# Optimization experiments

Measured on AMD Instinct MI355X. Metric: run time of the kernel, lower is better.

The kernel has to match this reference:

```python
import jax, jax.numpy as jnp
import numpy as np

N, E, F, DE, G, C = 50000, 800000, 64, 32, 512, 2
EPS = 1e-5


def setup_inputs() -> dict:
    key = jax.random.key(0)
    ks = jax.random.split(key, 12)
    Z = 2 * F + DE  # CGConv concat dim [x_i, x_j, edge_attr]
    inp = {
        "x": jax.random.normal(ks[0], (N, F), dtype=jnp.float32),
        "edge_index": jax.random.randint(ks[1], (2, E), 0, N, dtype=jnp.int32),
        "edge_attr": jax.random.normal(ks[2], (E, DE), dtype=jnp.float32),
        "batch": jnp.sort(jax.random.randint(ks[3], (N,), 0, G, dtype=jnp.int32)),
        # CGConv lin_f / lin_s : (2F+De) -> F, with bias
        "Wf": jax.random.normal(ks[4], (Z, F), dtype=jnp.float32) * 0.05,
        "bf": jnp.zeros((F,), dtype=jnp.float32),
        "Ws": jax.random.normal(ks[5], (Z, F), dtype=jnp.float32) * 0.05,
        "bs": jnp.zeros((F,), dtype=jnp.float32),
        # CGConv internal BatchNorm (training-mode batch stats)
        "bn_w": jnp.ones((F,), dtype=jnp.float32),
        "bn_b": jnp.zeros((F,), dtype=jnp.float32),
        # PyG LayerNorm (graph mode, batch=None -> whole-tensor stats)
        "ln_w": jnp.ones((F,), dtype=jnp.float32),
        "ln_b": jnp.zeros((F,), dtype=jnp.float32),
        # final linear (2F -> C) and output LayerNorm
        "Wl": jax.random.normal(ks[6], (2 * F, C), dtype=jnp.float32) * 0.05,
        "bl": jnp.zeros((C,), dtype=jnp.float32),
        "ln4_w": jnp.ones((C,), dtype=jnp.float32),
        "ln4_b": jnp.zeros((C,), dtype=jnp.float32),
    }
    return inp


def _pyg_layernorm(x, w, b):
    # torch_geometric.nn.LayerNorm, mode='graph', batch=None: whole-tensor stats
    xc = x - jnp.mean(x)
    out = xc / (jnp.sqrt(jnp.mean(xc * xc)) + EPS)
    return out * w + b


def reference(x, edge_index, edge_attr, batch, Wf, bf, Ws, bs, bn_w, bn_b,
              ln_w, ln_b, Wl, bl, ln4_w, ln4_b):
    src = edge_index[0]  # x_j (source)
    dst = edge_index[1]  # x_i (target / aggregation index)

    # CGConv message: sigmoid(lin_f(z)) * softplus(lin_s(z)), z=[x_i,x_j,e]
    z = jnp.concatenate([x[dst], x[src], edge_attr], axis=1)  # [E, 2F+De]
    msg = jax.nn.sigmoid(z @ Wf + bf) * jax.nn.softplus(z @ Ws + bs)  # [E,F]

    # scatter-add aggregation to target nodes
    agg = jax.ops.segment_sum(msg, dst, num_segments=N)  # [N,F]

    # CGConv batch_norm=True (training-mode batch statistics over nodes)
    mu = jnp.mean(agg, axis=0)
    var = jnp.mean((agg - mu) ** 2, axis=0)
    agg = (agg - mu) / jnp.sqrt(var + EPS) * bn_w + bn_b

    # residual
    h = agg + x

    # LayerNorm + softplus
    h = jax.nn.softplus(_pyg_layernorm(h, ln_w, ln_b))

    # global mean / add pooling over graphs
    add_pool = jax.ops.segment_sum(h, batch, num_segments=G)  # [G,F]
    counts = jax.ops.segment_sum(jnp.ones((N,), h.dtype), batch, num_segments=G)
    mean_pool = add_pool / jnp.maximum(counts, 1.0)[:, None]

    g = jnp.concatenate([mean_pool, add_pool], axis=1)  # [G, 2F]
    out = g @ Wl + bl  # [G, C]
    out = _pyg_layernorm(out, ln4_w, ln4_b)
    return out
```

## Files before the change

kernel.cpp:

```cpp
#include <hip/hip_runtime.h>
#include <math.h>

#define EPSF 1e-5f

typedef short bf16x8 __attribute__((ext_vector_type(8)));
typedef float f32x4 __attribute__((ext_vector_type(4)));

static __device__ __forceinline__ unsigned short f2bf(float x) {
  unsigned u = __float_as_uint(x);
  unsigned r = (u + 0x7FFFu + ((u >> 16) & 1u)) >> 16;
  return (unsigned short)r;
}

union BU { uint4 u; bf16x8 v; };

static __device__ __forceinline__ void gload16(const void* g, void* l) {
  __builtin_amdgcn_global_load_lds(
      (const __attribute__((address_space(1))) unsigned int*)g,
      (__attribute__((address_space(3))) unsigned int*)l, 16, 0, 0);
}

__global__ __launch_bounds__(256) void cvt_x(const float* __restrict__ x,
                                             unsigned short* __restrict__ xbf,
                                             int total8) {
  int i = blockIdx.x * 256 + threadIdx.x;
  if (i >= total8) return;
  float4 a = ((const float4*)x)[i * 2];
  float4 b = ((const float4*)x)[i * 2 + 1];
  unsigned short o[8];
  o[0] = f2bf(a.x); o[1] = f2bf(a.y); o[2] = f2bf(a.z); o[3] = f2bf(a.w);
  o[4] = f2bf(b.x); o[5] = f2bf(b.y); o[6] = f2bf(b.z); o[7] = f2bf(b.w);
  ((uint4*)xbf)[i] = *(uint4*)o;
}

__global__ __launch_bounds__(512) void bpack_kernel(
    const float* __restrict__ Wf, const float* __restrict__ Ws,
    unsigned short* __restrict__ Bfrag) {
  const int ks = blockIdx.x;
  const int t8 = threadIdx.x >> 6, l = threadIdx.x & 63;
  const int q = l & 15, g = l >> 4;
  const float* W = (t8 < 4) ? Wf : Ws;
  const int col = (t8 & 3) * 16 + q;
  unsigned short out[8];
#pragma unroll
  for (int i = 0; i < 8; ++i) {
    int r = ks * 32 + g * 8 + i;
    int wr = (r < 32) ? (128 + r) : (r - 32);
    out[i] = f2bf(W[(size_t)wr * 64 + col]);
  }
  *(uint4*)&Bfrag[((size_t)(ks * 8 + t8) * 64 + l) * 8] = *(uint4*)out;
}

__global__ void hist_kernel(const int* __restrict__ ei, int* __restrict__ deg,
                            int E) {
  int i = blockIdx.x * blockDim.x + threadIdx.x;
  if (i < E) atomicAdd(&deg[ei[E + i]], 1);
}

__global__ __launch_bounds__(256) void scan_a(const int* __restrict__ deg,
                                              int* __restrict__ bsum, int N) {
  const int idx = blockIdx.x * 256 + threadIdx.x;
  int v = (idx < N) ? deg[idx] : 0;
#pragma unroll
  for (int o = 32; o > 0; o >>= 1) v += __shfl_down(v, o);
  __shared__ int ws4[4];
  if ((threadIdx.x & 63) == 0) ws4[threadIdx.x >> 6] = v;
  __syncthreads();
  if (threadIdx.x == 0) bsum[blockIdx.x] = ws4[0] + ws4[1] + ws4[2] + ws4[3];
}

__global__ __launch_bounds__(256) void scan_b(const int* __restrict__ bsum,
                                              int* __restrict__ bpre, int NB) {
  const int t = threadIdx.x;
  const int lane = t & 63, w = t >> 6;
  int v = (t < NB) ? bsum[t] : 0;
  int sc = v;
#pragma unroll
  for (int o = 1; o < 64; o <<= 1) {
    int u = __shfl_up(sc, o);
    if (lane >= o) sc += u;
  }
  __shared__ int wsum[4];
  if (lane == 63) wsum[w] = sc;
  __syncthreads();
  int add = 0;
#pragma unroll
  for (int k = 0; k < 4; ++k) add += (k < w) ? wsum[k] : 0;
  bpre[t] = (sc - v) + add;
}

__global__ __launch_bounds__(256) void scan_c(const int* __restrict__ deg,
                                              const int* __restrict__ bpre,
                                              int* __restrict__ offsets,
                                              int* __restrict__ cursor, int N) {
  const int t = threadIdx.x;
  const int lane = t & 63, w = t >> 6;
  const int idx = blockIdx.x * 256 + t;
  int d = (idx < N) ? deg[idx] : 0;
  int sc = d;
#pragma unroll
  for (int o = 1; o < 64; o <<= 1) {
    int u = __shfl_up(sc, o);
    if (lane >= o) sc += u;
  }
  __shared__ int wsum[4];
  if (lane == 63) wsum[w] = sc;
  __syncthreads();
  int add = bpre[blockIdx.x];
#pragma unroll
  for (int k = 0; k < 4; ++k) add += (k < w) ? wsum[k] : 0;
  const int off = add + (sc - d);
  if (idx < N) {
    offsets[idx] = off;
    cursor[idx] = off;
    if (idx == N - 1) offsets[N] = off + d;
  }
}

__global__ void scatter_kernel(const int* __restrict__ ei,
                               int* __restrict__ cursor,
                               int4* __restrict__ epair4, int E) {
  int i = blockIdx.x * blockDim.x + threadIdx.x;
  if (i < E) {
    int dst = ei[E + i];
    int pos = atomicAdd(&cursor[dst], 1);
    epair4[pos] = make_int4(i, ei[i], dst, 0);
  }
}

__global__ __launch_bounds__(256) void edge_fused(
    const int4* __restrict__ epair4, const float* __restrict__ eattr,
    const unsigned short* __restrict__ xbf,
    const unsigned short* __restrict__ Bfrag, const float* __restrict__ bfv_,
    const float* __restrict__ bsv_, float* __restrict__ agg, int E, int N) {
  __shared__ __align__(16) unsigned short Ash[5][64][32];
  __shared__ __align__(16) int srcl[64];
  __shared__ __align__(16) int dstl[64];
  __shared__ __align__(16) int eidx[64];
  __shared__ __align__(4) unsigned char ridb[64];

  const int t = threadIdx.x, lane = t & 63, w = t >> 6;
  const int q = lane & 15, g = lane >> 4;
  const int base = blockIdx.x * 64;

  bf16x8 Bf[5], Bs[5];
#pragma unroll
  for (int ks = 0; ks < 5; ++ks) {
    BU u1, u2;
    u1.u = ((const uint4*)Bfrag)[(size_t)((ks * 8 + w) * 64 + lane)];
    u2.u = ((const uint4*)Bfrag)[(size_t)((ks * 8 + w + 4) * 64 + lane)];
    Bf[ks] = u1.v;
    Bs[ks] = u2.v;
  }
  const int feat = w * 16 + q;
  const float bfv = bfv_[feat];
  const float bsv = bsv_[feat];

  if (w == 0) {
    const int eg = base + lane;
    int4 p = make_int4(0, 0, 0x7FFFFFFF, 0);
    if (eg < E) p = epair4[eg];
    eidx[lane] = p.x;
    srcl[lane] = p.y;
    dstl[lane] = p.z;
    int d = p.z;
    int dprev = __shfl_up(d, 1);
    int flag = (lane == 0 || d != dprev) ? 1 : 0;
    int sc = flag;
#pragma unroll
    for (int o = 1; o < 64; o <<= 1) {
      int u = __shfl_up(sc, o);
      if (lane >= o) sc += u;
    }
    ridb[lane] = (unsigned char)(sc - 1);
  }
  __syncthreads();

  char* AshB = (char*)&Ash[0][0][0];
#pragma unroll
  for (int c2 = 0; c2 < 2; ++c2) {
    const int k = w + c2 * 4;
    const int row = 16 * (k & 3) + (lane >> 2);
    const int half = (k >> 2) * 32 + (lane & 3) * 8;
    int d = dstl[row];
    if ((unsigned)d >= (unsigned)N) d = 0;
    gload16(xbf + (size_t)d * 64 + half, AshB + 4096 + (size_t)k * 1024);
    const int s = srcl[row];
    gload16(xbf + (size_t)s * 64 + half, AshB + 12288 + (size_t)k * 1024);
  }

  {
    const int row = t >> 2, c = t & 3;
    const float* er = eattr + (size_t)eidx[row] * 32 + c * 8;
    float4 v0 = *(const float4*)er;
    float4 v1 = *(const float4*)(er + 4);
    bf16x8 sv;
    sv[0] = (short)f2bf(v0.x); sv[1] = (short)f2bf(v0.y);
    sv[2] = (short)f2bf(v0.z); sv[3] = (short)f2bf(v0.w);
    sv[4] = (short)f2bf(v1.x); sv[5] = (short)f2bf(v1.y);
    sv[6] = (short)f2bf(v1.z); sv[7] = (short)f2bf(v1.w);
    *(bf16x8*)&Ash[0][row][c * 8] = sv;
  }
  __syncthreads();

  f32x4 accf[4], accs[4];
#pragma unroll
  for (int mt = 0; mt < 4; ++mt) {
    accf[mt] = (f32x4){0.f, 0.f, 0.f, 0.f};
    accs[mt] = (f32x4){0.f, 0.f, 0.f, 0.f};
  }
#pragma unroll
  for (int ks = 0; ks < 5; ++ks) {
#pragma unroll
    for (int mt = 0; mt < 4; ++mt) {
      const bf16x8 a = *(const bf16x8*)&Ash[ks][mt * 16 + q][g * 8];
      accf[mt] =
          __builtin_amdgcn_mfma_f32_16x16x32_bf16(a, Bf[ks], accf[mt], 0, 0, 0);
      accs[mt] =
          __builtin_amdgcn_mfma_f32_16x16x32_bf16(a, Bs[ks], accs[mt], 0, 0, 0);
    }
  }

#pragma unroll
  for (int mt = 0; mt < 4; ++mt) {
    const int e0 = mt * 16 + g * 4;
    const unsigned rid4 = *(const unsigned*)&ridb[e0];
    const int4 d4 = *(const int4*)&dstl[e0];
    float m[4];
#pragma unroll
    for (int r = 0; r < 4; ++r) {
      float F = accf[mt][r] + bfv;
      float S = accs[mt][r] + bsv;
      float sig = __builtin_amdgcn_rcpf(1.0f + __expf(-F));
      float sp = fmaxf(S, 0.f) + __logf(1.0f + __expf(-fabsf(S)));
      m[r] = sig * sp;
    }
    const int r0 = rid4 & 255, r1 = (rid4 >> 8) & 255, r2 = (rid4 >> 16) & 255,
              r3 = rid4 >> 24;
    float a_ = m[0];
    int cur = r0, dc = d4.x;
    if (r1 == cur) a_ += m[1];
    else {
      if (dc < N) atomicAdd(&agg[(size_t)dc * 64 + feat], a_);
      cur = r1; dc = d4.y; a_ = m[1];
    }
    if (r2 == cur) a_ += m[2];
    else {
      if (dc < N) atomicAdd(&agg[(size_t)dc * 64 + feat], a_);
      cur = r2; dc = d4.z; a_ = m[2];
    }
    if (r3 == cur) a_ += m[3];
    else {
      if (dc < N) atomicAdd(&agg[(size_t)dc * 64 + feat], a_);
      cur = r3; dc = d4.w; a_ = m[3];
    }
    if (dc < N) atomicAdd(&agg[(size_t)dc * 64 + feat], a_);
  }
}

__global__ __launch_bounds__(256) void stats_kernel(
    const float* __restrict__ agg, const float* __restrict__ x,
    float* __restrict__ stats, int N) {
  const int f = threadIdx.x & 63;
  const int sub = threadIdx.x >> 6;
  float sa = 0, sa2 = 0, sx = 0, sx2 = 0, sax = 0;
  for (int r = blockIdx.x * 4 + sub; r < N; r += gridDim.x * 4) {
    float a = agg[(size_t)r * 64 + f];
    float xv = x[(size_t)r * 64 + f];
    sa += a; sa2 += a * a; sx += xv; sx2 += xv * xv; sax += a * xv;
  }
  __shared__ float lds[4][5][64];
  lds[sub][0][f] = sa; lds[sub][1][f] = sa2; lds[sub][2][f] = sx;
  lds[sub][3][f] = sx2; lds[sub][4][f] = sax;
  __syncthreads();
  if (sub == 0) {
#pragma unroll
    for (int i = 0; i < 5; ++i) {
      float v = lds[0][i][f] + lds[1][i][f] + lds[2][i][f] + lds[3][i][f];
      atomicAdd(&stats[i * 64 + f], v);
    }
  }
}

__global__ __launch_bounds__(256) void node_finish(
    const float* __restrict__ stats, const float* __restrict__ bn_w,
    const float* __restrict__ bn_b, const float* __restrict__ agg,
    const float* __restrict__ x, const int* __restrict__ batch,
    const float* __restrict__ ln_w, const float* __restrict__ ln_b,
    float* __restrict__ add_pool, float* __restrict__ counts, int N,
    int chunk) {
  const int f = threadIdx.x & 63;
  const int sub = threadIdx.x >> 6;
  const float Nf = (float)N;
  const float invN = 1.0f / Nf;
  float Sa = stats[f], Sa2 = stats[64 + f], Sx = stats[128 + f],
        Sx2 = stats[192 + f], Sax = stats[256 + f];
  float mu = Sa * invN;
  float var = Sa2 * invN - mu * mu;
  const float alpha = bn_w[f] / sqrtf(var + EPSF);
  const float beta = bn_b[f] - mu * alpha;
  float Sh = alpha * Sa + Nf * beta + Sx;
  float Sh2 = alpha * alpha * Sa2 + Sx2 + Nf * beta * beta +
              2.f * alpha * Sax + 2.f * alpha * beta * Sa + 2.f * beta * Sx;
#pragma unroll
  for (int o = 32; o > 0; o >>= 1) {
    Sh += __shfl_xor(Sh, o);
    Sh2 += __shfl_xor(Sh2, o);
  }
  const float cnt = Nf * 64.0f;
  const float mean = Sh / cnt;
  const float msq = Sh2 / cnt - mean * mean;
  const float rden = 1.0f / (sqrtf(fmaxf(msq, 0.f)) + EPSF);
  const float lw = ln_w[f] * rden;
  const float lb = ln_b[f];

  const int r0 = blockIdx.x * chunk;
  const int r1 = min(N, r0 + chunk);
  float acc = 0.f, cacc = 0.f;
  int curg = -1;
  for (int r = r0 + sub; r < r1; r += 4) {
    int g = batch[r];
    if (g != curg) {
      if (curg >= 0) {
        atomicAdd(&add_pool[(size_t)curg * 64 + f], acc);
        if (f == 0) atomicAdd(&counts[curg], cacc);
      }
      curg = g; acc = 0.f; cacc = 0.f;
    }
    float h = fmaf(alpha, agg[(size_t)r * 64 + f], beta) + x[(size_t)r * 64 + f];
    float v = (h - mean) * lw + lb;
    float sp = fmaxf(v, 0.f) + __logf(1.0f + __expf(-fabsf(v)));
    acc += sp; cacc += 1.f;
  }
  if (curg >= 0) {
    atomicAdd(&add_pool[(size_t)curg * 64 + f], acc);
    if (f == 0) atomicAdd(&counts[curg], cacc);
  }
}

__global__ __launch_bounds__(1024) void graph_out(
    const float* __restrict__ add_pool, const float* __restrict__ counts,
    const float* __restrict__ Wl, const float* __restrict__ bl,
    const float* __restrict__ w4, const float* __restrict__ b4,
    float* __restrict__ out, int G) {
  const int t = threadIdx.x;
  const int g = t >> 1, c = t & 1;
  float cnt = fmaxf(counts[g], 1.0f);
  float inv = 1.0f / cnt;
  const float4* ap4 = (const float4*)(add_pool + (size_t)g * 64);
  const float4* W4 = (const float4*)Wl;
  float v = bl[c];
#pragma unroll 4
  for (int k4 = 0; k4 < 16; ++k4) {
    float4 a4 = ap4[k4];
    float4 wa = W4[k4 * 2];
    float4 wb = W4[k4 * 2 + 1];
    float4 wc = W4[32 + k4 * 2];
    float4 wd = W4[32 + k4 * 2 + 1];
    float m0 = c ? wa.y : wa.x, m1 = c ? wa.w : wa.z;
    float m2 = c ? wb.y : wb.x, m3 = c ? wb.w : wb.z;
    float a0 = c ? wc.y : wc.x, a1 = c ? wc.w : wc.z;
    float a2 = c ? wd.y : wd.x, a3 = c ? wd.w : wd.z;
    v = fmaf(a4.x, fmaf(m0, inv, a0), v);
    v = fmaf(a4.y, fmaf(m1, inv, a1), v);
    v = fmaf(a4.z, fmaf(m2, inv, a2), v);
    v = fmaf(a4.w, fmaf(m3, inv, a3), v);
  }

  __shared__ float red[16];
  __shared__ float bc[2];
  float sum = v;
#pragma unroll
  for (int o = 32; o > 0; o >>= 1) sum += __shfl_down(sum, o);
  if ((t & 63) == 0) red[t >> 6] = sum;
  __syncthreads();
  if (t == 0) {
    float tot = 0;
#pragma unroll
    for (int i = 0; i < 16; ++i) tot += red[i];
    bc[0] = tot * (1.0f / 1024.0f);
  }
  __syncthreads();
  const float mean = bc[0];
  const float xc = v - mean;
  float sq = xc * xc;
  __syncthreads();
#pragma unroll
  for (int o = 32; o > 0; o >>= 1) sq += __shfl_down(sq, o);
  if ((t & 63) == 0) red[t >> 6] = sq;
  __syncthreads();
  if (t == 0) {
    float tot = 0;
#pragma unroll
    for (int i = 0; i < 16; ++i) tot += red[i];
    bc[1] = 1.0f / (sqrtf(tot * (1.0f / 1024.0f)) + EPSF);
  }
  __syncthreads();
  out[t] = xc * bc[1] * w4[c] + b4[c];
}

extern "C" void kernel_launch(void* const* d_in, const int* in_sizes, int n_in,
                              void* d_out, int out_size, void* d_ws,
                              size_t ws_size, hipStream_t stream) {
  const float* x = (const float*)d_in[0];
  const int* ei = (const int*)d_in[1];
  const float* eattr = (const float*)d_in[2];
  const int* batch = (const int*)d_in[3];
  const float* Wf = (const float*)d_in[4];
  const float* bf = (const float*)d_in[5];
  const float* Ws = (const float*)d_in[6];
  const float* bs = (const float*)d_in[7];
  const float* bn_w = (const float*)d_in[8];
  const float* bn_b = (const float*)d_in[9];
  const float* ln_w = (const float*)d_in[10];
  const float* ln_b = (const float*)d_in[11];
  const float* Wl = (const float*)d_in[12];
  const float* bl = (const float*)d_in[13];
  const float* w4 = (const float*)d_in[14];
  const float* b4 = (const float*)d_in[15];

  const int N = in_sizes[0] / 64;
  const int E = in_sizes[2] / 32;
  const int G = 512;
  const int NB = (N + 255) / 256;
  const int T = (E + 63) / 64;

  float* ws = (float*)d_ws;
  float* agg = ws;
  float* stats = agg + (size_t)N * 64;
  float* add_pool = stats + 320;
  float* counts = add_pool + (size_t)G * 64;
  int* deg = (int*)(counts + G);
  int* offsets = deg + N;
  int* cursor = offsets + N + 4;
  int* bsum = cursor + N;
  int* bpre = bsum + 256;
  unsigned short* Bfrag = (unsigned short*)(bpre + 256);
  unsigned short* xbf = Bfrag + 20480;
  int4* epair4 = (int4*)(xbf + (size_t)N * 64);

  size_t zeroFloats = (size_t)N * 64 + 320 + (size_t)G * 64 + G + N;
  hipMemsetAsync(agg, 0, zeroFloats * sizeof(float), stream);

  cvt_x<<<(N * 64 / 8 + 255) / 256, 256, 0, stream>>>(x, xbf, N * 64 / 8);
  bpack_kernel<<<5, 512, 0, stream>>>(Wf, Ws, Bfrag);
  hist_kernel<<<(E + 255) / 256, 256, 0, stream>>>(ei, deg, E);
  scan_a<<<NB, 256, 0, stream>>>(deg, bsum, N);
  scan_b<<<1, 256, 0, stream>>>(bsum, bpre, NB);
  scan_c<<<NB, 256, 0, stream>>>(deg, bpre, offsets, cursor, N);
  scatter_kernel<<<(E + 255) / 256, 256, 0, stream>>>(ei, cursor, epair4, E);
  edge_fused<<<T, 256, 0, stream>>>(epair4, eattr, xbf, Bfrag, bf, bs, agg, E,
                                    N);
  stats_kernel<<<512, 256, 0, stream>>>(agg, x, stats, N);
  const int chunk = (N + 511) / 512;
  node_finish<<<512, 256, 0, stream>>>(stats, bn_w, bn_b, agg, x, batch, ln_w,
                                       ln_b, add_pool, counts, N, chunk);
  graph_out<<<1, 1024, 0, stream>>>(add_pool, counts, Wl, bl, w4, b4,
                                    (float*)d_out, G);
}
```

Before: 328.7 us.

## Persistent double-buffered edge kernel with pre-sorted bf16 edge attributes and fused prep

Merges the x conversion, weight packing and degree histogram into one prep launch. The scatter step now writes edge attributes to bf16 in sorted order, so the edge kernel loads them contiguously with async LDS loads instead of gathering fp32 rows. The edge kernel becomes persistent with a fixed 768-block grid: each block walks a contiguous run of tiles and prefetches the next tile's metadata and operands into a second LDS buffer while computing the current one. It also adds an XOR swizzle to the LDS layout to avoid bank conflicts. In exchange it uses more LDS per block and adds extra scatter work, and it assumes node ids fit in 20 bits.

Result: no change. 329.2 us (+0.2%).

```diff
diff --git a/kernel.cpp b/kernel.cpp
--- a/kernel.cpp
+++ b/kernel.cpp
@@ -20,41 +20,42 @@
       (__attribute__((address_space(3))) unsigned int*)l, 16, 0, 0);
 }
 
-__global__ __launch_bounds__(256) void cvt_x(const float* __restrict__ x,
-                                             unsigned short* __restrict__ xbf,
-                                             int total8) {
-  int i = blockIdx.x * 256 + threadIdx.x;
-  if (i >= total8) return;
-  float4 a = ((const float4*)x)[i * 2];
-  float4 b = ((const float4*)x)[i * 2 + 1];
-  unsigned short o[8];
-  o[0] = f2bf(a.x); o[1] = f2bf(a.y); o[2] = f2bf(a.z); o[3] = f2bf(a.w);
-  o[4] = f2bf(b.x); o[5] = f2bf(b.y); o[6] = f2bf(b.z); o[7] = f2bf(b.w);
-  ((uint4*)xbf)[i] = *(uint4*)o;
-}
-
-__global__ __launch_bounds__(512) void bpack_kernel(
-    const float* __restrict__ Wf, const float* __restrict__ Ws,
-    unsigned short* __restrict__ Bfrag) {
-  const int ks = blockIdx.x;
-  const int t8 = threadIdx.x >> 6, l = threadIdx.x & 63;
-  const int q = l & 15, g = l >> 4;
-  const float* W = (t8 < 4) ? Wf : Ws;
-  const int col = (t8 & 3) * 16 + q;
-  unsigned short out[8];
-#pragma unroll
-  for (int i = 0; i < 8; ++i) {
-    int r = ks * 32 + g * 8 + i;
-    int wr = (r < 32) ? (128 + r) : (r - 32);
-    out[i] = f2bf(W[(size_t)wr * 64 + col]);
-  }
-  *(uint4*)&Bfrag[((size_t)(ks * 8 + t8) * 64 + l) * 8] = *(uint4*)out;
-}
-
-__global__ void hist_kernel(const int* __restrict__ ei, int* __restrict__ deg,
-                            int E) {
-  int i = blockIdx.x * blockDim.x + threadIdx.x;
-  if (i < E) atomicAdd(&deg[ei[E + i]], 1);
+__global__ __launch_bounds__(256) void prep_kernel(
+    const float* __restrict__ x, const float* __restrict__ Wf,
+    const float* __restrict__ Ws, const int* __restrict__ ei,
+    unsigned short* __restrict__ xbf, unsigned short* __restrict__ Bfrag,
+    int* __restrict__ deg, int NCV, int total8, int E) {
+  const int b = blockIdx.x, t = threadIdx.x;
+  if (b < NCV) {
+    int i = b * 256 + t;
+    if (i < total8) {
+      float4 a = ((const float4*)x)[i * 2];
+      float4 c = ((const float4*)x)[i * 2 + 1];
+      unsigned short o[8];
+      o[0] = f2bf(a.x); o[1] = f2bf(a.y); o[2] = f2bf(a.z); o[3] = f2bf(a.w);
+      o[4] = f2bf(c.x); o[5] = f2bf(c.y); o[6] = f2bf(c.z); o[7] = f2bf(c.w);
+      ((uint4*)xbf)[i] = *(uint4*)o;
+    }
+  } else if (b < NCV + 10) {
+    int g2 = (b - NCV) * 256 + t;
+    if (g2 < 2560) {
+      const int ks = g2 >> 9, t8 = (g2 >> 6) & 7, l = g2 & 63;
+      const int q = l & 15, g = l >> 4;
+      const float* W = (t8 < 4) ? Wf : Ws;
+      const int col = (t8 & 3) * 16 + q;
+      unsigned short out[8];
+#pragma unroll
+      for (int i = 0; i < 8; ++i) {
+        int r = ks * 32 + g * 8 + i;
+        int wr = (r < 32) ? (128 + r) : (r - 32);
+        out[i] = f2bf(W[(size_t)wr * 64 + col]);
+      }
+      *(uint4*)&Bfrag[((size_t)(ks * 8 + t8) * 64 + l) * 8] = *(uint4*)out;
+    }
+  } else {
+    int i = (b - NCV - 10) * 256 + t;
+    if (i < E) atomicAdd(&deg[ei[E + i]], 1);
+  }
 }
 
 __global__ __launch_bounds__(256) void scan_a(const int* __restrict__ deg,
@@ -91,7 +92,6 @@
 
 __global__ __launch_bounds__(256) void scan_c(const int* __restrict__ deg,
                                               const int* __restrict__ bpre,
-                                              int* __restrict__ offsets,
                                               int* __restrict__ cursor, int N) {
   const int t = threadIdx.x;
   const int lane = t & 63, w = t >> 6;
@@ -109,152 +109,170 @@
   int add = bpre[blockIdx.x];
 #pragma unroll
   for (int k = 0; k < 4; ++k) add += (k < w) ? wsum[k] : 0;
-  const int off = add + (sc - d);
-  if (idx < N) {
-    offsets[idx] = off;
-    cursor[idx] = off;
-    if (idx == N - 1) offsets[N] = off + d;
-  }
-}
-
-__global__ void scatter_kernel(const int* __restrict__ ei,
-                               int* __restrict__ cursor,
-                               int4* __restrict__ epair4, int E) {
-  int i = blockIdx.x * blockDim.x + threadIdx.x;
-  if (i < E) {
-    int dst = ei[E + i];
-    int pos = atomicAdd(&cursor[dst], 1);
-    epair4[pos] = make_int4(i, ei[i], dst, 0);
-  }
-}
-
-__global__ __launch_bounds__(256) void edge_fused(
-    const int4* __restrict__ epair4, const float* __restrict__ eattr,
+  if (idx < N) cursor[idx] = add + (sc - d);
+}
+
+__global__ __launch_bounds__(256) void scatter_pack(
+    const int* __restrict__ ei, int* __restrict__ cursor,
+    const float* __restrict__ eattr, int2* __restrict__ epair2,
+    unsigned short* __restrict__ eabf, int E) {
+  int i = blockIdx.x * 256 + threadIdx.x;
+  if (i >= E) return;
+  const int dst = ei[E + i];
+  const int pos = atomicAdd(&cursor[dst], 1);
+  epair2[pos] = make_int2(ei[i], dst);
+  const float4* er = (const float4*)(eattr + (size_t)i * 32);
+  unsigned short o[32];
+#pragma unroll
+  for (int k = 0; k < 8; ++k) {
+    float4 v = er[k];
+    o[k * 4] = f2bf(v.x); o[k * 4 + 1] = f2bf(v.y);
+    o[k * 4 + 2] = f2bf(v.z); o[k * 4 + 3] = f2bf(v.w);
+  }
+  uint4* dp = (uint4*)(eabf + (size_t)pos * 32);
+#pragma unroll
+  for (int k = 0; k < 4; ++k) dp[k] = ((uint4*)o)[k];
+}
+
+__global__ __launch_bounds__(256, 3) void edge_fused(
+    const int2* __restrict__ epair2, const unsigned short* __restrict__ eabf,
     const unsigned short* __restrict__ xbf,
     const unsigned short* __restrict__ Bfrag, const float* __restrict__ bfv_,
-    const float* __restrict__ bsv_, float* __restrict__ agg, int E, int N) {
-  __shared__ __align__(16) unsigned short Ash[5][64][32];
-  __shared__ __align__(16) int srcl[64];
-  __shared__ __align__(16) int dstl[64];
-  __shared__ __align__(16) int eidx[64];
-  __shared__ __align__(4) unsigned char ridb[64];
-
-  const int t = threadIdx.x, lane = t & 63, w = t >> 6;
+    const float* __restrict__ bsv_, float* __restrict__ agg, int T, int N) {
+  __shared__ __align__(16) unsigned char AshB[40960];
+  __shared__ __align__(16) int metaLDS[128];
+
+  const int tt = threadIdx.x, lane = tt & 63, w = tt >> 6;
   const int q = lane & 15, g = lane >> 4;
-  const int base = blockIdx.x * 64;
+
+  const int nB = gridDim.x;
+  const int c = (blockIdx.x & 7) * (nB >> 3) + (blockIdx.x >> 3);
+  const int q8 = T / nB, r8 = T - q8 * nB;
+  const int t0 = c * q8 + min(c, r8);
+  const int t1 = t0 + q8 + (c < r8 ? 1 : 0);
+  if (t0 >= t1) return;
 
   bf16x8 Bf[5], Bs[5];
 #pragma unroll
   for (int ks = 0; ks < 5; ++ks) {
     BU u1, u2;
-    u1.u = ((const uint4*)Bfrag)[(size_t)((ks * 8 + w) * 64 + lane)];
-    u2.u = ((const uint4*)Bfrag)[(size_t)((ks * 8 + w + 4) * 64 + lane)];
-    Bf[ks] = u1.v;
-    Bs[ks] = u2.v;
+    u1.u = ((const uint4*)Bfrag)[(ks * 8 + w) * 64 + lane];
+    u2.u = ((const uint4*)Bfrag)[(ks * 8 + w + 4) * 64 + lane];
+    Bf[ks] = u1.v; Bs[ks] = u2.v;
   }
   const int feat = w * 16 + q;
-  const float bfv = bfv_[feat];
-  const float bsv = bsv_[feat];
-
-  if (w == 0) {
-    const int eg = base + lane;
-    int4 p = make_int4(0, 0, 0x7FFFFFFF, 0);
-    if (eg < E) p = epair4[eg];
-    eidx[lane] = p.x;
-    srcl[lane] = p.y;
-    dstl[lane] = p.z;
-    int d = p.z;
-    int dprev = __shfl_up(d, 1);
-    int flag = (lane == 0 || d != dprev) ? 1 : 0;
+  const float bfv = bfv_[feat], bsv = bsv_[feat];
+
+  int mSrc = 0, mDst = 0, nSrc = 0, nDst = 0;
+
+  auto META = [&](int tile, int& S, int& D, int pbN) {
+    int2 p = epair2[(size_t)tile * 64 + lane];
+    S = p.x; D = p.y;
+    int dp = __shfl_up(D, 1);
+    int flag = (lane == 0 || D != dp) ? 1 : 0;
     int sc = flag;
 #pragma unroll
     for (int o = 1; o < 64; o <<= 1) {
       int u = __shfl_up(sc, o);
       if (lane >= o) sc += u;
     }
-    ridb[lane] = (unsigned char)(sc - 1);
-  }
-  __syncthreads();
-
-  char* AshB = (char*)&Ash[0][0][0];
-#pragma unroll
-  for (int c2 = 0; c2 < 2; ++c2) {
-    const int k = w + c2 * 4;
-    const int row = 16 * (k & 3) + (lane >> 2);
-    const int half = (k >> 2) * 32 + (lane & 3) * 8;
-    int d = dstl[row];
-    if ((unsigned)d >= (unsigned)N) d = 0;
-    gload16(xbf + (size_t)d * 64 + half, AshB + 4096 + (size_t)k * 1024);
-    const int s = srcl[row];
-    gload16(xbf + (size_t)s * 64 + half, AshB + 12288 + (size_t)k * 1024);
-  }
-
-  {
-    const int row = t >> 2, c = t & 3;
-    const float* er = eattr + (size_t)eidx[row] * 32 + c * 8;
-    float4 v0 = *(const float4*)er;
-    float4 v1 = *(const float4*)(er + 4);
-    bf16x8 sv;
-    sv[0] = (short)f2bf(v0.x); sv[1] = (short)f2bf(v0.y);
-    sv[2] = (short)f2bf(v0.z); sv[3] = (short)f2bf(v0.w);
-    sv[4] = (short)f2bf(v1.x); sv[5] = (short)f2bf(v1.y);
-    sv[6] = (short)f2bf(v1.z); sv[7] = (short)f2bf(v1.w);
-    *(bf16x8*)&Ash[0][row][c * 8] = sv;
-  }
-  __syncthreads();
-
-  f32x4 accf[4], accs[4];
-#pragma unroll
-  for (int mt = 0; mt < 4; ++mt) {
-    accf[mt] = (f32x4){0.f, 0.f, 0.f, 0.f};
-    accs[mt] = (f32x4){0.f, 0.f, 0.f, 0.f};
-  }
-#pragma unroll
-  for (int ks = 0; ks < 5; ++ks) {
+    if (w == 0) metaLDS[pbN * 64 + lane] = ((sc - 1) << 20) | (D & 0xFFFFF);
+  };
+
+  auto STAGE = [&](int tile, int bufB, int S, int D) {
+    const int row = (w << 4) + (lane >> 2);
+    const int cx = (lane & 3) ^ ((row >> 1) & 3);
+    int dR = __shfl(D, row);
+    int sR = __shfl(S, row);
+    unsigned du = ((unsigned)dR < (unsigned)N) ? (unsigned)dR : 0u;
+    unsigned su = ((unsigned)sR < (unsigned)N) ? (unsigned)sR : 0u;
+    gload16(eabf + (size_t)tile * 2048 + row * 32 + cx * 8,
+            AshB + bufB + w * 1024);
+    gload16(xbf + (size_t)du * 64 + cx * 8, AshB + bufB + 4096 + w * 1024);
+    gload16(xbf + (size_t)du * 64 + 32 + cx * 8,
+            AshB + bufB + 4096 + (w + 4) * 1024);
+    gload16(xbf + (size_t)su * 64 + cx * 8, AshB + bufB + 12288 + w * 1024);
+    gload16(xbf + (size_t)su * 64 + 32 + cx * 8,
+            AshB + bufB + 12288 + (w + 4) * 1024);
+  };
+
+  META(t0, mSrc, mDst, 0);
+  STAGE(t0, 0, mSrc, mDst);
+  int pb = 0;
+  for (int t = t0; t < t1; ++t) {
+    const int bufC = pb * 20480;
+    if (t + 1 < t1) {
+      META(t + 1, nSrc, nDst, pb ^ 1);
+      STAGE(t + 1, 20480 - bufC, nSrc, nDst);
+    } else {
+      asm volatile("s_waitcnt vmcnt(0)" ::: "memory");
+    }
+    asm volatile("s_waitcnt lgkmcnt(0)" ::: "memory");
+    __builtin_amdgcn_sched_barrier(0);
+    __builtin_amdgcn_s_barrier();
+    __builtin_amdgcn_sched_barrier(0);
+
+    f32x4 accf[4], accs[4];
 #pragma unroll
     for (int mt = 0; mt < 4; ++mt) {
-      const bf16x8 a = *(const bf16x8*)&Ash[ks][mt * 16 + q][g * 8];
-      accf[mt] =
-          __builtin_amdgcn_mfma_f32_16x16x32_bf16(a, Bf[ks], accf[mt], 0, 0, 0);
-      accs[mt] =
-          __builtin_amdgcn_mfma_f32_16x16x32_bf16(a, Bs[ks], accs[mt], 0, 0, 0);
-    }
-  }
-
-#pragma unroll
-  for (int mt = 0; mt < 4; ++mt) {
-    const int e0 = mt * 16 + g * 4;
-    const unsigned rid4 = *(const unsigned*)&ridb[e0];
-    const int4 d4 = *(const int4*)&dstl[e0];
-    float m[4];
-#pragma unroll
-    for (int r = 0; r < 4; ++r) {
-      float F = accf[mt][r] + bfv;
-      float S = accs[mt][r] + bsv;
-      float sig = __builtin_amdgcn_rcpf(1.0f + __expf(-F));
-      float sp = fmaxf(S, 0.f) + __logf(1.0f + __expf(-fabsf(S)));
-      m[r] = sig * sp;
-    }
-    const int r0 = rid4 & 255, r1 = (rid4 >> 8) & 255, r2 = (rid4 >> 16) & 255,
-              r3 = rid4 >> 24;
-    float a_ = m[0];
-    int cur = r0, dc = d4.x;
-    if (r1 == cur) a_ += m[1];
-    else {
-      if (dc < N) atomicAdd(&agg[(size_t)dc * 64 + feat], a_);
-      cur = r1; dc = d4.y; a_ = m[1];
-    }
-    if (r2 == cur) a_ += m[2];
-    else {
-      if (dc < N) atomicAdd(&agg[(size_t)dc * 64 + feat], a_);
-      cur = r2; dc = d4.z; a_ = m[2];
-    }
-    if (r3 == cur) a_ += m[3];
-    else {
-      if (dc < N) atomicAdd(&agg[(size_t)dc * 64 + feat], a_);
-      cur = r3; dc = d4.w; a_ = m[3];
-    }
-    if (dc < N) atomicAdd(&agg[(size_t)dc * 64 + feat], a_);
+      accf[mt] = (f32x4){0.f, 0.f, 0.f, 0.f};
+      accs[mt] = (f32x4){0.f, 0.f, 0.f, 0.f};
+    }
+#pragma unroll
+    for (int ks = 0; ks < 5; ++ks) {
+#pragma unroll
+      for (int mt = 0; mt < 4; ++mt) {
+        const int row = mt * 16 + q;
+        const int ch = g ^ ((row >> 1) & 3);
+        const bf16x8 a =
+            *(const bf16x8*)(AshB + bufC + ks * 4096 + row * 64 + ch * 16);
+        accf[mt] = __builtin_amdgcn_mfma_f32_16x16x32_bf16(a, Bf[ks],
+                                                           accf[mt], 0, 0, 0);
+        accs[mt] = __builtin_amdgcn_mfma_f32_16x16x32_bf16(a, Bs[ks],
+                                                           accs[mt], 0, 0, 0);
+      }
+    }
+
+#pragma unroll
+    for (int mt = 0; mt < 4; ++mt) {
+      const int e0 = mt * 16 + g * 4;
+      const uint4 mw = *(const uint4*)&metaLDS[pb * 64 + e0];
+      float mm[4];
+#pragma unroll
+      for (int r = 0; r < 4; ++r) {
+        float F = accf[mt][r] + bfv;
+        float S = accs[mt][r] + bsv;
+        float sig = __builtin_amdgcn_rcpf(1.0f + __expf(-F));
+        float sp = fmaxf(S, 0.f) + __logf(1.0f + __expf(-fabsf(S)));
+        mm[r] = sig * sp;
+      }
+      const unsigned u0 = mw.x, u1 = mw.y, u2 = mw.z, u3 = mw.w;
+      const unsigned d0 = u0 & 0xFFFFFu, d1 = u1 & 0xFFFFFu,
+                     d2 = u2 & 0xFFFFFu, d3 = u3 & 0xFFFFFu;
+      const unsigned r0 = u0 >> 20, r1 = u1 >> 20, r2 = u2 >> 20, r3 = u3 >> 20;
+      float a_ = mm[0];
+      unsigned cur = r0, dc = d0;
+      if (r1 == cur) a_ += mm[1];
+      else {
+        if (dc < (unsigned)N) atomicAdd(&agg[(size_t)dc * 64 + feat], a_);
+        cur = r1; dc = d1; a_ = mm[1];
+      }
+      if (r2 == cur) a_ += mm[2];
+      else {
+        if (dc < (unsigned)N) atomicAdd(&agg[(size_t)dc * 64 + feat], a_);
+        cur = r2; dc = d2; a_ = mm[2];
+      }
+      if (r3 == cur) a_ += mm[3];
+      else {
+        if (dc < (unsigned)N) atomicAdd(&agg[(size_t)dc * 64 + feat], a_);
+        cur = r3; dc = d3; a_ = mm[3];
+      }
+      if (dc < (unsigned)N) atomicAdd(&agg[(size_t)dc * 64 + feat], a_);
+    }
+
+    mSrc = nSrc; mDst = nDst;
+    pb ^= 1;
+    __builtin_amdgcn_s_barrier();
   }
 }
 
@@ -424,6 +442,8 @@
   const int G = 512;
   const int NB = (N + 255) / 256;
   const int T = (E + 63) / 64;
+  const int NCV = (N * 8 + 255) / 256;
+  const int NH = (E + 255) / 256;
 
   float* ws = (float*)d_ws;
   float* agg = ws;
@@ -431,26 +451,27 @@
   float* add_pool = stats + 320;
   float* counts = add_pool + (size_t)G * 64;
   int* deg = (int*)(counts + G);
-  int* offsets = deg + N;
-  int* cursor = offsets + N + 4;
+  int* cursor = deg + N;
   int* bsum = cursor + N;
   int* bpre = bsum + 256;
   unsigned short* Bfrag = (unsigned short*)(bpre + 256);
   unsigned short* xbf = Bfrag + 20480;
-  int4* epair4 = (int4*)(xbf + (size_t)N * 64);
+  unsigned short* eabf = xbf + (size_t)N * 64;
+  int2* epair2 = (int2*)(eabf + (size_t)T * 2048);
 
   size_t zeroFloats = (size_t)N * 64 + 320 + (size_t)G * 64 + G + N;
   hipMemsetAsync(agg, 0, zeroFloats * sizeof(float), stream);
-
-  cvt_x<<<(N * 64 / 8 + 255) / 256, 256, 0, stream>>>(x, xbf, N * 64 / 8);
-  bpack_kernel<<<5, 512, 0, stream>>>(Wf, Ws, Bfrag);
-  hist_kernel<<<(E + 255) / 256, 256, 0, stream>>>(ei, deg, E);
+  const int padE = T * 64 - E;
+  if (padE > 0) hipMemsetAsync(epair2 + E, 0xFF, (size_t)padE * 8, stream);
+
+  prep_kernel<<<NCV + 10 + NH, 256, 0, stream>>>(x, Wf, Ws, ei, xbf, Bfrag,
+                                                 deg, NCV, N * 8, E);
   scan_a<<<NB, 256, 0, stream>>>(deg, bsum, N);
   scan_b<<<1, 256, 0, stream>>>(bsum, bpre, NB);
-  scan_c<<<NB, 256, 0, stream>>>(deg, bpre, offsets, cursor, N);
-  scatter_kernel<<<(E + 255) / 256, 256, 0, stream>>>(ei, cursor, epair4, E);
-  edge_fused<<<T, 256, 0, stream>>>(epair4, eattr, xbf, Bfrag, bf, bs, agg, E,
-                                    N);
+  scan_c<<<NB, 256, 0, stream>>>(deg, bpre, cursor, N);
+  scatter_pack<<<NH, 256, 0, stream>>>(ei, cursor, eattr, epair2, eabf, E);
+  edge_fused<<<768, 256, 0, stream>>>(epair2, eabf, xbf, Bfrag, bf, bs, agg, T,
+                                      N);
   stats_kernel<<<512, 256, 0, stream>>>(agg, x, stats, N);
   const int chunk = (N + 511) / 512;
   node_finish<<<512, 256, 0, stream>>>(stats, bn_w, bn_b, agg, x, batch, ln_w,
```

## Merge prep kernels and restructure edge gather with swizzled LDS and early loads

Applied to the files above, without the earlier changes.

Folds the x bf16 conversion, weight-fragment packing and degree histogram into one multi-role launch, and drops the unused offsets array. In the edge kernel, each thread now reads its own edge record and issues the x-row and edge-attribute gathers before the weight-fragment loads and the first barrier, which removes one barrier and the LDS index arrays. LDS A-tiles use an XOR swizzle on the 16-byte chunks to cut bank conflicts. The tail of the sorted edge array is padded with 0xFF via memset so out-of-range edges are skipped by unsigned bounds checks.

After: 320.2 us. -2.6%, faster.

```diff
diff --git a/kernel.cpp b/kernel.cpp
--- a/kernel.cpp
+++ b/kernel.cpp
@@ -12,6 +12,12 @@
   return (unsigned short)r;
 }
 
+static __device__ __forceinline__ float msgv(float F, float S) {
+  float sig = __builtin_amdgcn_rcpf(1.0f + __expf(-F));
+  float sp = fmaxf(S, 0.f) + __logf(1.0f + __expf(-fabsf(S)));
+  return sig * sp;
+}
+
 union BU { uint4 u; bf16x8 v; };
 
 static __device__ __forceinline__ void gload16(const void* g, void* l) {
@@ -20,41 +26,42 @@
       (__attribute__((address_space(3))) unsigned int*)l, 16, 0, 0);
 }
 
-__global__ __launch_bounds__(256) void cvt_x(const float* __restrict__ x,
-                                             unsigned short* __restrict__ xbf,
-                                             int total8) {
-  int i = blockIdx.x * 256 + threadIdx.x;
-  if (i >= total8) return;
-  float4 a = ((const float4*)x)[i * 2];
-  float4 b = ((const float4*)x)[i * 2 + 1];
-  unsigned short o[8];
-  o[0] = f2bf(a.x); o[1] = f2bf(a.y); o[2] = f2bf(a.z); o[3] = f2bf(a.w);
-  o[4] = f2bf(b.x); o[5] = f2bf(b.y); o[6] = f2bf(b.z); o[7] = f2bf(b.w);
-  ((uint4*)xbf)[i] = *(uint4*)o;
-}
-
-__global__ __launch_bounds__(512) void bpack_kernel(
-    const float* __restrict__ Wf, const float* __restrict__ Ws,
-    unsigned short* __restrict__ Bfrag) {
-  const int ks = blockIdx.x;
-  const int t8 = threadIdx.x >> 6, l = threadIdx.x & 63;
-  const int q = l & 15, g = l >> 4;
-  const float* W = (t8 < 4) ? Wf : Ws;
-  const int col = (t8 & 3) * 16 + q;
-  unsigned short out[8];
-#pragma unroll
-  for (int i = 0; i < 8; ++i) {
-    int r = ks * 32 + g * 8 + i;
-    int wr = (r < 32) ? (128 + r) : (r - 32);
-    out[i] = f2bf(W[(size_t)wr * 64 + col]);
-  }
-  *(uint4*)&Bfrag[((size_t)(ks * 8 + t8) * 64 + l) * 8] = *(uint4*)out;
-}
-
-__global__ void hist_kernel(const int* __restrict__ ei, int* __restrict__ deg,
-                            int E) {
-  int i = blockIdx.x * blockDim.x + threadIdx.x;
-  if (i < E) atomicAdd(&deg[ei[E + i]], 1);
+__global__ __launch_bounds__(256) void prep_kernel(
+    const float* __restrict__ x, const float* __restrict__ Wf,
+    const float* __restrict__ Ws, const int* __restrict__ ei,
+    unsigned short* __restrict__ xbf, unsigned short* __restrict__ Bfrag,
+    int* __restrict__ deg, int NCV, int total8, int E) {
+  const int b = blockIdx.x, t = threadIdx.x;
+  if (b < NCV) {
+    int i = b * 256 + t;
+    if (i < total8) {
+      float4 a = ((const float4*)x)[i * 2];
+      float4 c = ((const float4*)x)[i * 2 + 1];
+      unsigned short o[8];
+      o[0] = f2bf(a.x); o[1] = f2bf(a.y); o[2] = f2bf(a.z); o[3] = f2bf(a.w);
+      o[4] = f2bf(c.x); o[5] = f2bf(c.y); o[6] = f2bf(c.z); o[7] = f2bf(c.w);
+      ((uint4*)xbf)[i] = *(uint4*)o;
+    }
+  } else if (b < NCV + 10) {
+    int g2 = (b - NCV) * 256 + t;
+    if (g2 < 2560) {
+      const int ks = g2 >> 9, t8 = (g2 >> 6) & 7, l = g2 & 63;
+      const int q = l & 15, g = l >> 4;
+      const float* W = (t8 < 4) ? Wf : Ws;
+      const int col = (t8 & 3) * 16 + q;
+      unsigned short out[8];
+#pragma unroll
+      for (int i = 0; i < 8; ++i) {
+        int kk = ks * 32 + g * 8 + i;
+        int wr = (kk < 32) ? (128 + kk) : (kk - 32);
+        out[i] = f2bf(W[(size_t)wr * 64 + col]);
+      }
+      *(uint4*)&Bfrag[((size_t)(ks * 8 + t8) * 64 + l) * 8] = *(uint4*)out;
+    }
+  } else {
+    int i = (b - NCV - 10) * 256 + t;
+    if (i < E) atomicAdd(&deg[ei[E + i]], 1);
+  }
 }
 
 __global__ __launch_bounds__(256) void scan_a(const int* __restrict__ deg,
@@ -91,7 +98,6 @@
 
 __global__ __launch_bounds__(256) void scan_c(const int* __restrict__ deg,
                                               const int* __restrict__ bpre,
-                                              int* __restrict__ offsets,
                                               int* __restrict__ cursor, int N) {
   const int t = threadIdx.x;
   const int lane = t & 63, w = t >> 6;
@@ -109,23 +115,17 @@
   int add = bpre[blockIdx.x];
 #pragma unroll
   for (int k = 0; k < 4; ++k) add += (k < w) ? wsum[k] : 0;
-  const int off = add + (sc - d);
-  if (idx < N) {
-    offsets[idx] = off;
-    cursor[idx] = off;
-    if (idx == N - 1) offsets[N] = off + d;
-  }
+  if (idx < N) cursor[idx] = add + (sc - d);
 }
 
 __global__ void scatter_kernel(const int* __restrict__ ei,
                                int* __restrict__ cursor,
                                int4* __restrict__ epair4, int E) {
-  int i = blockIdx.x * blockDim.x + threadIdx.x;
-  if (i < E) {
-    int dst = ei[E + i];
-    int pos = atomicAdd(&cursor[dst], 1);
-    epair4[pos] = make_int4(i, ei[i], dst, 0);
-  }
+  int i = blockIdx.x * 256 + threadIdx.x;
+  if (i >= E) return;
+  int dst = ei[E + i];
+  int pos = atomicAdd(&cursor[dst], 1);
+  epair4[pos] = make_int4(i, ei[i], dst, 0);
 }
 
 __global__ __launch_bounds__(256) void edge_fused(
@@ -134,64 +134,32 @@
     const unsigned short* __restrict__ Bfrag, const float* __restrict__ bfv_,
     const float* __restrict__ bsv_, float* __restrict__ agg, int E, int N) {
   __shared__ __align__(16) unsigned short Ash[5][64][32];
-  __shared__ __align__(16) int srcl[64];
   __shared__ __align__(16) int dstl[64];
-  __shared__ __align__(16) int eidx[64];
   __shared__ __align__(4) unsigned char ridb[64];
 
   const int t = threadIdx.x, lane = t & 63, w = t >> 6;
   const int q = lane & 15, g = lane >> 4;
   const int base = blockIdx.x * 64;
 
-  bf16x8 Bf[5], Bs[5];
-#pragma unroll
-  for (int ks = 0; ks < 5; ++ks) {
-    BU u1, u2;
-    u1.u = ((const uint4*)Bfrag)[(size_t)((ks * 8 + w) * 64 + lane)];
-    u2.u = ((const uint4*)Bfrag)[(size_t)((ks * 8 + w + 4) * 64 + lane)];
-    Bf[ks] = u1.v;
-    Bs[ks] = u2.v;
-  }
-  const int feat = w * 16 + q;
-  const float bfv = bfv_[feat];
-  const float bsv = bsv_[feat];
-
-  if (w == 0) {
-    const int eg = base + lane;
-    int4 p = make_int4(0, 0, 0x7FFFFFFF, 0);
-    if (eg < E) p = epair4[eg];
-    eidx[lane] = p.x;
-    srcl[lane] = p.y;
-    dstl[lane] = p.z;
-    int d = p.z;
-    int dprev = __shfl_up(d, 1);
-    int flag = (lane == 0 || d != dprev) ? 1 : 0;
-    int sc = flag;
-#pragma unroll
-    for (int o = 1; o < 64; o <<= 1) {
-      int u = __shfl_up(sc, o);
-      if (lane >= o) sc += u;
-    }
-    ridb[lane] = (unsigned char)(sc - 1);
-  }
-  __syncthreads();
-
-  char* AshB = (char*)&Ash[0][0][0];
-#pragma unroll
-  for (int c2 = 0; c2 < 2; ++c2) {
-    const int k = w + c2 * 4;
-    const int row = 16 * (k & 3) + (lane >> 2);
-    const int half = (k >> 2) * 32 + (lane & 3) * 8;
-    int d = dstl[row];
-    if ((unsigned)d >= (unsigned)N) d = 0;
-    gload16(xbf + (size_t)d * 64 + half, AshB + 4096 + (size_t)k * 1024);
-    const int s = srcl[row];
-    gload16(xbf + (size_t)s * 64 + half, AshB + 12288 + (size_t)k * 1024);
-  }
+  const int myrow = w * 16 + (lane >> 2);
+  const int c = lane & 3;
+  const int4 p4 = epair4[base + myrow];
+  const int sw = (myrow >> 1) & 3;
+  const int cs = c ^ sw;
 
   {
-    const int row = t >> 2, c = t & 3;
-    const float* er = eattr + (size_t)eidx[row] * 32 + c * 8;
+    unsigned du = ((unsigned)p4.z < (unsigned)N) ? (unsigned)p4.z : 0u;
+    unsigned su = ((unsigned)p4.y < (unsigned)N) ? (unsigned)p4.y : 0u;
+    char* AshB = (char*)&Ash[0][0][0];
+    gload16(xbf + (size_t)du * 64 + cs * 8, AshB + 4096 + w * 1024);
+    gload16(xbf + (size_t)du * 64 + 32 + cs * 8, AshB + 4096 + (w + 4) * 1024);
+    gload16(xbf + (size_t)su * 64 + cs * 8, AshB + 12288 + w * 1024);
+    gload16(xbf + (size_t)su * 64 + 32 + cs * 8, AshB + 12288 + (w + 4) * 1024);
+  }
+
+  {
+    unsigned exi = ((unsigned)p4.x < (unsigned)E) ? (unsigned)p4.x : 0u;
+    const float* er = eattr + (size_t)exi * 32 + cs * 8;
     float4 v0 = *(const float4*)er;
     float4 v1 = *(const float4*)(er + 4);
     bf16x8 sv;
@@ -199,7 +167,35 @@
     sv[2] = (short)f2bf(v0.z); sv[3] = (short)f2bf(v0.w);
     sv[4] = (short)f2bf(v1.x); sv[5] = (short)f2bf(v1.y);
     sv[6] = (short)f2bf(v1.z); sv[7] = (short)f2bf(v1.w);
-    *(bf16x8*)&Ash[0][row][c * 8] = sv;
+    *(bf16x8*)&Ash[0][myrow][c * 8] = sv;
+  }
+
+  bf16x8 Bf[5], Bs[5];
+#pragma unroll
+  for (int ks = 0; ks < 5; ++ks) {
+    BU u1, u2;
+    u1.u = ((const uint4*)Bfrag)[(size_t)((ks * 8 + w) * 64 + lane)];
+    u2.u = ((const uint4*)Bfrag)[(size_t)((ks * 8 + w + 4) * 64 + lane)];
+    Bf[ks] = u1.v;
+    Bs[ks] = u2.v;
+  }
+  const int feat = w * 16 + q;
+  const float bfv = bfv_[feat];
+  const float bsv = bsv_[feat];
+
+  if (w == 0) {
+    const int4 pp = epair4[base + lane];
+    dstl[lane] = pp.z;
+    int d = pp.z;
+    int dprev = __shfl_up(d, 1);
+    int flag = (lane == 0 || d != dprev) ? 1 : 0;
+    int sc = flag;
+#pragma unroll
+    for (int o = 1; o < 64; o <<= 1) {
+      int u = __shfl_up(sc, o);
+      if (lane >= o) sc += u;
+    }
+    ridb[lane] = (unsigned char)(sc - 1);
   }
   __syncthreads();
 
@@ -213,7 +209,9 @@
   for (int ks = 0; ks < 5; ++ks) {
 #pragma unroll
     for (int mt = 0; mt < 4; ++mt) {
-      const bf16x8 a = *(const bf16x8*)&Ash[ks][mt * 16 + q][g * 8];
+      const int row = mt * 16 + q;
+      const int ch = g ^ ((row >> 1) & 3);
+      const bf16x8 a = *(const bf16x8*)&Ash[ks][row][ch * 8];
       accf[mt] =
           __builtin_amdgcn_mfma_f32_16x16x32_bf16(a, Bf[ks], accf[mt], 0, 0, 0);
       accs[mt] =
@@ -231,9 +229,7 @@
     for (int r = 0; r < 4; ++r) {
       float F = accf[mt][r] + bfv;
       float S = accs[mt][r] + bsv;
-      float sig = __builtin_amdgcn_rcpf(1.0f + __expf(-F));
-      float sp = fmaxf(S, 0.f) + __logf(1.0f + __expf(-fabsf(S)));
-      m[r] = sig * sp;
+      m[r] = msgv(F, S);
     }
     const int r0 = rid4 & 255, r1 = (rid4 >> 8) & 255, r2 = (rid4 >> 16) & 255,
               r3 = rid4 >> 24;
@@ -241,20 +237,20 @@
     int cur = r0, dc = d4.x;
     if (r1 == cur) a_ += m[1];
     else {
-      if (dc < N) atomicAdd(&agg[(size_t)dc * 64 + feat], a_);
+      if ((unsigned)dc < (unsigned)N) atomicAdd(&agg[(size_t)dc * 64 + feat], a_);
       cur = r1; dc = d4.y; a_ = m[1];
     }
     if (r2 == cur) a_ += m[2];
     else {
-      if (dc < N) atomicAdd(&agg[(size_t)dc * 64 + feat], a_);
+      if ((unsigned)dc < (unsigned)N) atomicAdd(&agg[(size_t)dc * 64 + feat], a_);
       cur = r2; dc = d4.z; a_ = m[2];
     }
     if (r3 == cur) a_ += m[3];
     else {
-      if (dc < N) atomicAdd(&agg[(size_t)dc * 64 + feat], a_);
+      if ((unsigned)dc < (unsigned)N) atomicAdd(&agg[(size_t)dc * 64 + feat], a_);
       cur = r3; dc = d4.w; a_ = m[3];
     }
-    if (dc < N) atomicAdd(&agg[(size_t)dc * 64 + feat], a_);
+    if ((unsigned)dc < (unsigned)N) atomicAdd(&agg[(size_t)dc * 64 + feat], a_);
   }
 }
 
@@ -424,6 +420,8 @@
   const int G = 512;
   const int NB = (N + 255) / 256;
   const int T = (E + 63) / 64;
+  const int NCV = (N * 8 + 255) / 256;
+  const int NH = (E + 255) / 256;
 
   float* ws = (float*)d_ws;
   float* agg = ws;
@@ -431,8 +429,7 @@
   float* add_pool = stats + 320;
   float* counts = add_pool + (size_t)G * 64;
   int* deg = (int*)(counts + G);
-  int* offsets = deg + N;
-  int* cursor = offsets + N + 4;
+  int* cursor = deg + N;
   int* bsum = cursor + N;
   int* bpre = bsum + 256;
   unsigned short* Bfrag = (unsigned short*)(bpre + 256);
@@ -441,14 +438,15 @@
 
   size_t zeroFloats = (size_t)N * 64 + 320 + (size_t)G * 64 + G + N;
   hipMemsetAsync(agg, 0, zeroFloats * sizeof(float), stream);
-
-  cvt_x<<<(N * 64 / 8 + 255) / 256, 256, 0, stream>>>(x, xbf, N * 64 / 8);
-  bpack_kernel<<<5, 512, 0, stream>>>(Wf, Ws, Bfrag);
-  hist_kernel<<<(E + 255) / 256, 256, 0, stream>>>(ei, deg, E);
+  const int padE = T * 64 - E;
+  if (padE > 0) hipMemsetAsync(epair4 + E, 0xFF, (size_t)padE * 16, stream);
+
+  prep_kernel<<<NCV + 10 + NH, 256, 0, stream>>>(x, Wf, Ws, ei, xbf, Bfrag,
+                                                 deg, NCV, N * 8, E);
   scan_a<<<NB, 256, 0, stream>>>(deg, bsum, N);
   scan_b<<<1, 256, 0, stream>>>(bsum, bpre, NB);
-  scan_c<<<NB, 256, 0, stream>>>(deg, bpre, offsets, cursor, N);
-  scatter_kernel<<<(E + 255) / 256, 256, 0, stream>>>(ei, cursor, epair4, E);
+  scan_c<<<NB, 256, 0, stream>>>(deg, bpre, cursor, N);
+  scatter_kernel<<<NH, 256, 0, stream>>>(ei, cursor, epair4, E);
   edge_fused<<<T, 256, 0, stream>>>(epair4, eattr, xbf, Bfrag, bf, bs, agg, E,
                                     N);
   stats_kernel<<<512, 256, 0, stream>>>(agg, x, stats, N);
```
